# Optimization experiments

Hardware: AMD Instinct MI355X
Metric: run time of the kernel (lower is better)

Reference implementation:

```python
import jax, jax.numpy as jnp
import numpy as np

B, S, D, E, O = 1024, 256, 512, 16, 512


def setup_inputs() -> dict:
    key = jax.random.key(0)
    k_x, k_wg, k_bg, k_we, k_be = jax.random.split(key, 5)
    scale_g = 1.0 / np.sqrt(D)
    scale_e = 1.0 / np.sqrt(D)
    return {
        "x": jax.random.normal(k_x, (B, S, D), dtype=jnp.float32),
        # gating linear: Linear(D, E)
        "Wg": jax.random.uniform(k_wg, (D, E), jnp.float32, -scale_g, scale_g),
        "bg": jax.random.uniform(k_bg, (E,), jnp.float32, -scale_g, scale_g),
        # experts: E stacked Linear(D, O) weights (stored as [E, D, O], i.e. W.T per expert)
        "We": jax.random.uniform(k_we, (E, D, O), jnp.float32, -scale_e, scale_e),
        "be": jax.random.uniform(k_be, (E, O), jnp.float32, -scale_e, scale_e),
    }


def reference(x, Wg, bg, We, be):
    # scorer: mean over non-batch dims -> linear -> softmax
    scores = jax.nn.softmax(jnp.mean(x, axis=1) @ Wg + bg, axis=-1)  # [B, E]
    idx = jnp.argmax(scores, axis=-1)                                 # [B]
    gate = jnp.take_along_axis(scores, idx[:, None], axis=-1)         # [B, 1]
    # top-1 dispatch: gather each sample's expert weights, one batched GEMM
    W_sel = We[idx]                                                   # [B, D, O]
    b_sel = be[idx]                                                   # [B, O]
    y = jnp.einsum('bsd,bdo->bso', x, W_sel) + b_sel[:, None, :]      # [B, S, O]
    return gate[:, :, None] * y
```

## Files before the change

### kernel.cpp

```cpp
#include <hip/hip_runtime.h>
#include <hip/hip_bf16.h>
#include <math.h>

#define B 1024
#define S 256
#define D 512
#define E 16
#define O 512

typedef __bf16 bf16x8 __attribute__((ext_vector_type(8)));
typedef float f32x4 __attribute__((ext_vector_type(4)));
typedef unsigned short u16x4 __attribute__((ext_vector_type(4)));
typedef unsigned short u16x8 __attribute__((ext_vector_type(8)));

__device__ inline unsigned short f2bf(float f) {
    unsigned int u = __float_as_uint(f);
    unsigned int r = u + 0x7FFFu + ((u >> 16) & 1u);
    return (unsigned short)(r >> 16);
}

__global__ __launch_bounds__(256) void cast_transpose_We(
    const float* __restrict__ We, unsigned short* __restrict__ Wt)
{
    const int bid = blockIdx.x;
    const int ot = bid & 15;
    const int dt = (bid >> 4) & 15;
    const int e  = bid >> 8;

    __shared__ unsigned short tile[32][33];

    const int r  = threadIdx.x >> 3;
    const int c4 = (threadIdx.x & 7) * 4;

    const float* src = We + (((size_t)e * D + dt * 32 + r) * O + ot * 32 + c4);
    float4 v = *(const float4*)src;
    tile[r][c4 + 0] = f2bf(v.x);
    tile[r][c4 + 1] = f2bf(v.y);
    tile[r][c4 + 2] = f2bf(v.z);
    tile[r][c4 + 3] = f2bf(v.w);
    __syncthreads();

    u16x4 w;
    w.x = tile[c4 + 0][r];
    w.y = tile[c4 + 1][r];
    w.z = tile[c4 + 2][r];
    w.w = tile[c4 + 3][r];
    unsigned short* dst = Wt + (((size_t)e * O + ot * 32 + r) * D + dt * 32 + c4);
    *(u16x4*)dst = w;
}

__global__ __launch_bounds__(256) void gate_kernel(
    const float* __restrict__ x, const float* __restrict__ Wg,
    const float* __restrict__ bg, float* __restrict__ gatep,
    int* __restrict__ idxp)
{
    const int b = blockIdx.x;
    const int t = threadIdx.x;

    const int h  = t >> 7;
    const int d4 = (t & 127) * 4;

    const float* xb = x + (size_t)b * S * D + d4;
    float ax = 0.f, ay = 0.f, az = 0.f, aw = 0.f;
    #pragma unroll 8
    for (int s = h * 128; s < h * 128 + 128; ++s) {
        float4 v = *(const float4*)(xb + (size_t)s * D);
        ax += v.x; ay += v.y; az += v.z; aw += v.w;
    }

    __shared__ float ms2[2][D];
    ms2[h][d4 + 0] = ax;
    ms2[h][d4 + 1] = ay;
    ms2[h][d4 + 2] = az;
    ms2[h][d4 + 3] = aw;
    __syncthreads();

    const float sx = ms2[0][2 * t]     + ms2[1][2 * t];
    const float sy = ms2[0][2 * t + 1] + ms2[1][2 * t + 1];
    const float* wg0 = Wg + (size_t)(2 * t) * E;
    const float* wg1 = Wg + (size_t)(2 * t + 1) * E;
    float part[E];
    #pragma unroll
    for (int e = 0; e < E; ++e) part[e] = sx * wg0[e] + sy * wg1[e];

    #pragma unroll
    for (int e = 0; e < E; ++e) {
        float v = part[e];
        for (int off = 32; off > 0; off >>= 1) v += __shfl_down(v, off);
        part[e] = v;
    }

    __shared__ float wred[4][E];
    const int wave = t >> 6, lane = t & 63;
    if (lane == 0) {
        #pragma unroll
        for (int e = 0; e < E; ++e) wred[wave][e] = part[e];
    }
    __syncthreads();

    if (t == 0) {
        float logits[E];
        #pragma unroll
        for (int e = 0; e < E; ++e)
            logits[e] = (wred[0][e] + wred[1][e] + wred[2][e] + wred[3][e])
                            * (1.0f / (float)S) + bg[e];
        float m = logits[0];
        int am = 0;
        #pragma unroll
        for (int e = 1; e < E; ++e)
            if (logits[e] > m) { m = logits[e]; am = e; }
        float sum = 0.f;
        #pragma unroll
        for (int e = 0; e < E; ++e) sum += expf(logits[e] - m);
        gatep[b] = 1.0f / sum;
        idxp[b]  = am;
    }
}

__global__ __launch_bounds__(256) void moe_gemm(
    const float* __restrict__ x, const unsigned short* __restrict__ Wt,
    const float* __restrict__ be, const float* __restrict__ gatep,
    const int* __restrict__ idxp, float* __restrict__ out)
{
    const int bid = blockIdx.x;
    const int nt = bid & 3;
    const int mt = (bid >> 2) & 1;
    const int b  = bid >> 3;
    const int m0 = mt * 128;
    const int n0 = nt * 128;

    const int t    = threadIdx.x;
    const int lane = t & 63;
    const int wave = t >> 6;
    const int wr   = wave >> 1;
    const int wc   = wave & 1;

    const int   e    = idxp[b];
    const float gate = gatep[b];

    __shared__ unsigned short As[128 * 32];
    __shared__ unsigned short Bs[128 * 32];

    const float*          Ab = x  + ((size_t)b * S + m0) * D;
    const unsigned short* Bb = Wt + ((size_t)e * O + n0) * D;

    f32x4 acc[4][4];
    #pragma unroll
    for (int i = 0; i < 4; ++i)
        #pragma unroll
        for (int j = 0; j < 4; ++j)
            #pragma unroll
            for (int r = 0; r < 4; ++r) acc[i][j][r] = 0.0f;

    for (int kk = 0; kk < D; kk += 32) {
        __syncthreads();

        #pragma unroll
        for (int i = 0; i < 2; ++i) {
            const int c  = i * 256 + t;
            const int n  = c >> 2;
            const int k8 = (c & 3) * 8;
            u16x8 w = *(const u16x8*)(Bb + (size_t)n * D + kk + k8);
            *(u16x8*)&Bs[c * 8] = w;
        }
        #pragma unroll
        for (int i = 0; i < 4; ++i) {
            const int c  = i * 256 + t;
            const int m  = c >> 3;
            const int k4 = (c & 7) * 4;
            float4 v = *(const float4*)(Ab + (size_t)m * D + kk + k4);
            u16x4 w;
            w.x = f2bf(v.x); w.y = f2bf(v.y); w.z = f2bf(v.z); w.w = f2bf(v.w);
            *(u16x4*)&As[m * 32 + k4] = w;
        }
        __syncthreads();

        bf16x8 fa[4], fb[4];
        #pragma unroll
        for (int i = 0; i < 4; ++i) {
            const int r = wr * 64 + i * 16 + (lane & 15);
            fa[i] = *(const bf16x8*)&As[r * 32 + (lane >> 4) * 8];
            const int n = wc * 64 + i * 16 + (lane & 15);
            fb[i] = *(const bf16x8*)&Bs[n * 32 + (lane >> 4) * 8];
        }
        #pragma unroll
        for (int i = 0; i < 4; ++i)
            #pragma unroll
            for (int j = 0; j < 4; ++j)
                acc[i][j] = __builtin_amdgcn_mfma_f32_16x16x32_bf16(
                    fa[i], fb[j], acc[i][j], 0, 0, 0);
    }

    float* ob = out + (size_t)b * S * O;
    #pragma unroll
    for (int j = 0; j < 4; ++j) {
        const int col  = n0 + wc * 64 + j * 16 + (lane & 15);
        const float bias = be[(size_t)e * O + col];
        #pragma unroll
        for (int i = 0; i < 4; ++i) {
            const int row0 = m0 + wr * 64 + i * 16 + (lane >> 4) * 4;
            #pragma unroll
            for (int r = 0; r < 4; ++r)
                ob[(size_t)(row0 + r) * O + col] = gate * (acc[i][j][r] + bias);
        }
    }
}

extern "C" void kernel_launch(void* const* d_in, const int* in_sizes, int n_in,
                              void* d_out, int out_size, void* d_ws, size_t ws_size,
                              hipStream_t stream) {
    const float* x  = (const float*)d_in[0];
    const float* Wg = (const float*)d_in[1];
    const float* bg = (const float*)d_in[2];
    const float* We = (const float*)d_in[3];
    const float* be = (const float*)d_in[4];
    float* out = (float*)d_out;

    unsigned short* Wt = (unsigned short*)d_ws;
    float* gatep = (float*)((char*)d_ws + (size_t)E * O * D * sizeof(unsigned short));
    int*   idxp  = (int*)((char*)gatep + B * sizeof(float));

    cast_transpose_We<<<E * (D / 32) * (O / 32), 256, 0, stream>>>(We, Wt);
    gate_kernel<<<B, 256, 0, stream>>>(x, Wg, bg, gatep, idxp);
    moe_gemm<<<B * 8, 256, 0, stream>>>(x, Wt, be, gatep, idxp, out);
}
```

Measured before the change: 1.226 ms.

## Split gating column reduction, swizzle GEMM block order, use native bf16 convert

Splits the gating mean reduction into a two-block-per-sample partial-sum kernel plus a finish kernel, doubling parallelism for the bandwidth-bound pass over x, with partials staged in the output buffer. Remaps GEMM block indices so consecutive blocks span different samples and tiles, changing L2 locality and expert-weight reuse patterns. Replaces the manual float-to-bf16 rounding with native __bf16 conversion for the A tile. Adds an extra kernel launch and relies on the output buffer as scratch before the GEMM overwrites it.

```diff
diff --git a/kernel.cpp b/kernel.cpp
--- a/kernel.cpp
+++ b/kernel.cpp
@@ -1,5 +1,4 @@
 #include <hip/hip_runtime.h>
-#include <hip/hip_bf16.h>
 #include <math.h>
 
 #define B 1024
@@ -9,6 +8,7 @@
 #define O 512
 
 typedef __bf16 bf16x8 __attribute__((ext_vector_type(8)));
+typedef __bf16 bf16x4 __attribute__((ext_vector_type(4)));
 typedef float f32x4 __attribute__((ext_vector_type(4)));
 typedef unsigned short u16x4 __attribute__((ext_vector_type(4)));
 typedef unsigned short u16x8 __attribute__((ext_vector_type(8)));
@@ -49,34 +49,52 @@
     *(u16x4*)dst = w;
 }
 
-__global__ __launch_bounds__(256) void gate_kernel(
-    const float* __restrict__ x, const float* __restrict__ Wg,
+__global__ __launch_bounds__(256) void col_partial(
+    const float* __restrict__ x, float* __restrict__ partial)
+{
+    const int blk = blockIdx.x;
+    const int p   = blk & 1;
+    const int b   = blk >> 1;
+    const int t   = threadIdx.x;
+    const int h   = t >> 7;
+    const int d4  = (t & 127) * 4;
+
+    const int s0 = p * 128 + h * 64;
+    const float* xb = x + ((size_t)b * S + s0) * D + d4;
+
+    float ax = 0.f, ay = 0.f, az = 0.f, aw = 0.f;
+    #pragma unroll 16
+    for (int s = 0; s < 64; ++s) {
+        float4 v = *(const float4*)(xb + (size_t)s * D);
+        ax += v.x; ay += v.y; az += v.z; aw += v.w;
+    }
+
+    __shared__ float red[D];
+    if (h == 1) {
+        red[d4 + 0] = ax; red[d4 + 1] = ay; red[d4 + 2] = az; red[d4 + 3] = aw;
+    }
+    __syncthreads();
+    if (h == 0) {
+        float4 o;
+        o.x = ax + red[d4 + 0];
+        o.y = ay + red[d4 + 1];
+        o.z = az + red[d4 + 2];
+        o.w = aw + red[d4 + 3];
+        *(float4*)(partial + (((size_t)b * 2 + p) * D + d4)) = o;
+    }
+}
+
+__global__ __launch_bounds__(256) void gate_finish(
+    const float* __restrict__ partial, const float* __restrict__ Wg,
     const float* __restrict__ bg, float* __restrict__ gatep,
     int* __restrict__ idxp)
 {
     const int b = blockIdx.x;
     const int t = threadIdx.x;
 
-    const int h  = t >> 7;
-    const int d4 = (t & 127) * 4;
-
-    const float* xb = x + (size_t)b * S * D + d4;
-    float ax = 0.f, ay = 0.f, az = 0.f, aw = 0.f;
-    #pragma unroll 8
-    for (int s = h * 128; s < h * 128 + 128; ++s) {
-        float4 v = *(const float4*)(xb + (size_t)s * D);
-        ax += v.x; ay += v.y; az += v.z; aw += v.w;
-    }
-
-    __shared__ float ms2[2][D];
-    ms2[h][d4 + 0] = ax;
-    ms2[h][d4 + 1] = ay;
-    ms2[h][d4 + 2] = az;
-    ms2[h][d4 + 3] = aw;
-    __syncthreads();
-
-    const float sx = ms2[0][2 * t]     + ms2[1][2 * t];
-    const float sy = ms2[0][2 * t + 1] + ms2[1][2 * t + 1];
+    const float* pb = partial + (size_t)b * 2 * D;
+    const float sx = pb[2 * t]     + pb[D + 2 * t];
+    const float sy = pb[2 * t + 1] + pb[D + 2 * t + 1];
     const float* wg0 = Wg + (size_t)(2 * t) * E;
     const float* wg1 = Wg + (size_t)(2 * t + 1) * E;
     float part[E];
@@ -122,7 +140,8 @@
     const float* __restrict__ be, const float* __restrict__ gatep,
     const int* __restrict__ idxp, float* __restrict__ out)
 {
-    const int bid = blockIdx.x;
+    const int bid0 = blockIdx.x;
+    const int bid  = ((bid0 & 7) << 10) | (bid0 >> 3);
     const int nt = bid & 3;
     const int mt = (bid >> 2) & 1;
     const int b  = bid >> 3;
@@ -169,9 +188,10 @@
             const int m  = c >> 3;
             const int k4 = (c & 7) * 4;
             float4 v = *(const float4*)(Ab + (size_t)m * D + kk + k4);
-            u16x4 w;
-            w.x = f2bf(v.x); w.y = f2bf(v.y); w.z = f2bf(v.z); w.w = f2bf(v.w);
-            *(u16x4*)&As[m * 32 + k4] = w;
+            bf16x4 w;
+            w.x = (__bf16)v.x; w.y = (__bf16)v.y;
+            w.z = (__bf16)v.z; w.w = (__bf16)v.w;
+            *(bf16x4*)&As[m * 32 + k4] = w;
         }
         __syncthreads();
 
@@ -220,7 +240,10 @@
     float* gatep = (float*)((char*)d_ws + (size_t)E * O * D * sizeof(unsigned short));
     int*   idxp  = (int*)((char*)gatep + B * sizeof(float));
 
+    float* partial = out;
+
     cast_transpose_We<<<E * (D / 32) * (O / 32), 256, 0, stream>>>(We, Wt);
-    gate_kernel<<<B, 256, 0, stream>>>(x, Wg, bg, gatep, idxp);
+    col_partial<<<B * 2, 256, 0, stream>>>(x, partial);
+    gate_finish<<<B, 256, 0, stream>>>(partial, Wg, bg, gatep, idxp);
     moe_gemm<<<B * 8, 256, 0, stream>>>(x, Wt, be, gatep, idxp, out);
 }
```

Measured after the change: 1.203 ms. No clear change (-1.8%).
